# Kernel tuning notes

Hardware: AMD Instinct MI355X
Metric: run time of the kernel (lower is better)

The kernel has to match this reference:

```python
import jax, jax.numpy as jnp
import numpy as np

B_, L, D = 4, 2048, 1024          # batch, seq_len, d_model
E = 2 * D                         # d_inner (expand=2)
N = 8                             # d_state
K = 4                             # d_conv
R = D // 16                       # dt_rank = 64
EPS = 1e-5


def silu(x):
    return x * jax.nn.sigmoid(x)


def setup_inputs() -> dict:
    key = jax.random.key(0)
    ks = jax.random.split(key, 8)
    s = 0.02
    inp = jax.random.normal(ks[0], (B_, L, D), jnp.float32)
    in_proj_w = jax.random.normal(ks[1], (2 * E, D), jnp.float32) * s
    conv_w = jax.random.normal(ks[2], (E, 1, K), jnp.float32) * s  # depthwise, OIW
    conv_b = jnp.zeros((E,), jnp.float32)
    x_proj_w = jax.random.normal(ks[3], (R + 2 * N, E), jnp.float32) * s
    dt_proj_w = jax.random.normal(ks[4], (E, R), jnp.float32) * s
    # bias so softplus(dt) gives realistic small timesteps
    dt_proj_b = jax.random.uniform(ks[5], (E,), jnp.float32, minval=-4.0, maxval=-2.0)
    # S4D-real init: A = -[1..N] per channel
    A_log = jnp.log(jnp.broadcast_to(jnp.arange(1, N + 1, dtype=jnp.float32), (E, N)))
    D_param = jnp.ones((E,), jnp.float32)
    out_proj_w = jax.random.normal(ks[6], (D, E), jnp.float32) * s
    rms_w = jnp.ones((D,), jnp.float32)
    return dict(inp=inp, in_proj_w=in_proj_w, conv_w=conv_w, conv_b=conv_b,
                x_proj_w=x_proj_w, dt_proj_w=dt_proj_w, dt_proj_b=dt_proj_b,
                A_log=A_log, D_param=D_param, out_proj_w=out_proj_w, rms_w=rms_w)


def reference(inp, in_proj_w, conv_w, conv_b, x_proj_w, dt_proj_w, dt_proj_b,
              A_log, D_param, out_proj_w, rms_w):
    b, l, d = inp.shape
    # input projection -> x (ssm branch) and z (gate branch), each (b, l, E)
    xz = inp @ in_proj_w.T
    x, z = jnp.split(xz, 2, axis=-1)
    # depthwise causal conv1d along time
    xt = x.transpose(0, 2, 1)                                   # (b, E, l)
    xc = jax.lax.conv_general_dilated(xt, conv_w, (1,), [(K - 1, 0)],
                                      feature_group_count=E)
    x = silu((xc + conv_b[None, :, None]).transpose(0, 2, 1))   # (b, l, E)
    # data-dependent SSM params
    dbc = x @ x_proj_w.T                                        # (b, l, R+2N)
    dt, Bm, Cm = jnp.split(dbc, [R, R + N], axis=-1)
    delta = jax.nn.softplus(dt @ dt_proj_w.T + dt_proj_b)       # (b, l, E)
    A = -jnp.exp(A_log)                                         # (E, N)

    def step(h, t):
        d_t, B_t, C_t, u_t = t                                  # (b,E),(b,N),(b,N),(b,E)
        dA = jnp.exp(d_t[..., None] * A)                        # (b, E, N)
        h = h * dA + (d_t * u_t)[..., None] * B_t[:, None, :]
        y = jnp.einsum('ben,bn->be', h, C_t)
        return h, y

    xs = (delta.transpose(1, 0, 2), Bm.transpose(1, 0, 2),
          Cm.transpose(1, 0, 2), x.transpose(1, 0, 2))
    h0 = jnp.zeros((b, E, N), inp.dtype)
    _, ys = jax.lax.scan(step, h0, xs)                          # ys: (l, b, E)
    y = ys.transpose(1, 0, 2) + x * D_param                     # skip term u*D
    y = y * silu(z)                                             # gating
    out = y @ out_proj_w.T                                      # (b, l, D)
    # RMSNorm
    out = out * jax.lax.rsqrt(jnp.mean(out * out, axis=-1, keepdims=True) + EPS) * rms_w
    # dropout p=0 -> identity
    return out
```

## Files before the change

### kernel.cpp

```cpp
#include <hip/hip_runtime.h>

#define LL 2048
#define EE 2048
#define DD 1024
#define NC 64
#define CH 32

typedef short bf16x8 __attribute__((ext_vector_type(8)));
typedef float f32x4 __attribute__((ext_vector_type(4)));

__device__ inline float bf2f(unsigned short u) {
    union { unsigned u; float f; } v; v.u = ((unsigned)u) << 16; return v.f;
}
__device__ inline unsigned short f2bf(float f) {
    union { float f; unsigned u; } v; v.f = f;
    unsigned r = v.u + 0x7fff + ((v.u >> 16) & 1);
    return (unsigned short)(r >> 16);
}

__device__ inline void gload_lds16(const void* g, void* lds) {
    __builtin_amdgcn_global_load_lds(
        (const __attribute__((address_space(1))) unsigned int*)g,
        (__attribute__((address_space(3))) unsigned int*)lds, 16, 0, 0);
}

template<int MODE, int BN>
__global__ __launch_bounds__(512, 2)
void gemm4p(const unsigned short* __restrict__ A,
            const unsigned short* __restrict__ Bw,
            void* __restrict__ Cout,
            const float* __restrict__ bias,
            int M, int N, int K)
{
    constexpr int NREP = BN / 64;
    constexpr int RB   = BN / 128;
    constexpr int LH   = 2 + RB;
    constexpr int NSTRIP = BN / 4;

    extern __shared__ short lds[];
    short* Asm = lds;
    short* Bsm = lds + 2 * 2 * 256 * 32;

    const int tid = threadIdx.x;
    const int w = tid >> 6, lane = tid & 63;
    const int wm = w >> 2, wn = w & 3;

    const int gx = N / BN;
    const int nwg = gx * (M / 256);
    int lin = blockIdx.y * gx + blockIdx.x;
    int swz = ((nwg & 7) == 0) ? ((lin & 7) * (nwg >> 3) + (lin >> 3)) : lin;
    const long m0 = (long)(swz / gx) * 256;
    const long n0 = (long)(swz % gx) * BN;

    const int g = (tid & 3) ^ ((tid >> 3) & 3);
    const int arow = tid >> 2;
    const unsigned short* Ag = A + (m0 + arow) * (long)K + g * 8;
    const unsigned short* Bg = Bw + (n0 + arow) * (long)K + g * 8;
    const int ldsrow = w * 16;

    auto stageA = [&](int buf, int kh, int j, int kt) {
        gload_lds16(Ag + (long)j * 128 * K + kt * 64 + kh * 32,
                    Asm + ((buf * 2 + kh) * 256 + j * 128 + ldsrow) * 32);
    };
    auto stageB = [&](int buf, int kh, int j, int kt) {
        gload_lds16(Bg + (long)j * 128 * K + kt * 64 + kh * 32,
                    Bsm + ((buf * 2 + kh) * BN + j * 128 + ldsrow) * 32);
    };

    f32x4 acc[8][NREP] = {};

    stageA(0, 0, 0, 0); stageA(0, 0, 1, 0);
#pragma unroll
    for (int j = 0; j < RB; ++j) stageB(0, 0, j, 0);
    stageA(0, 1, 0, 0); stageA(0, 1, 1, 0);
#pragma unroll
    for (int j = 0; j < RB; ++j) stageB(0, 1, j, 0);
    asm volatile("s_waitcnt vmcnt(%0)" :: "i"(LH) : "memory");
    __builtin_amdgcn_s_barrier();

    const int NT = K / 64;
    const int rr = lane & 15;
    const int sl = ((lane >> 4) ^ ((rr >> 1) & 3)) * 8;

    for (int t = 0; t < NT; ++t) {
        const int cur = t & 1, nxt = cur ^ 1;
        const bool more = (t + 1 < NT);
        const short* Ac0 = Asm + (cur * 2 + 0) * 256 * 32;
        const short* Bc0 = Bsm + (cur * 2 + 0) * BN * 32;
        const short* Ac1 = Asm + (cur * 2 + 1) * 256 * 32;
        const short* Bc1 = Bsm + (cur * 2 + 1) * BN * 32;
        bf16x8 a[4], b[NREP];

#pragma unroll
        for (int n = 0; n < NREP; ++n)
            b[n] = *(const bf16x8*)&Bc0[(wn * NSTRIP + n * 16 + rr) * 32 + sl];
#pragma unroll
        for (int m = 0; m < 4; ++m)
            a[m] = *(const bf16x8*)&Ac0[(wm * 128 + m * 16 + rr) * 32 + sl];
        if (more) { stageA(nxt, 0, 0, t + 1); stageA(nxt, 0, 1, t + 1); }
        __builtin_amdgcn_s_barrier();
        asm volatile("s_waitcnt lgkmcnt(0)" ::: "memory");
        __builtin_amdgcn_sched_barrier(0);
        __builtin_amdgcn_s_setprio(1);
#pragma unroll
        for (int m = 0; m < 4; ++m)
#pragma unroll
            for (int n = 0; n < NREP; ++n)
                acc[m][n] = __builtin_amdgcn_mfma_f32_16x16x32_bf16(a[m], b[n], acc[m][n], 0, 0, 0);
        __builtin_amdgcn_s_setprio(0);
        __builtin_amdgcn_s_barrier();

#pragma unroll
        for (int m = 0; m < 4; ++m)
            a[m] = *(const bf16x8*)&Ac0[(wm * 128 + 64 + m * 16 + rr) * 32 + sl];
        if (more) {
#pragma unroll
            for (int j = 0; j < RB; ++j) stageB(nxt, 0, j, t + 1);
            asm volatile("s_waitcnt vmcnt(%0)" :: "i"(LH) : "memory");
        } else {
            asm volatile("s_waitcnt vmcnt(0)" ::: "memory");
        }
        __builtin_amdgcn_s_barrier();
        asm volatile("s_waitcnt lgkmcnt(0)" ::: "memory");
        __builtin_amdgcn_sched_barrier(0);
        __builtin_amdgcn_s_setprio(1);
#pragma unroll
        for (int m = 0; m < 4; ++m)
#pragma unroll
            for (int n = 0; n < NREP; ++n)
                acc[4 + m][n] = __builtin_amdgcn_mfma_f32_16x16x32_bf16(a[m], b[n], acc[4 + m][n], 0, 0, 0);
        __builtin_amdgcn_s_setprio(0);
        __builtin_amdgcn_s_barrier();

#pragma unroll
        for (int n = 0; n < NREP; ++n)
            b[n] = *(const bf16x8*)&Bc1[(wn * NSTRIP + n * 16 + rr) * 32 + sl];
#pragma unroll
        for (int m = 0; m < 4; ++m)
            a[m] = *(const bf16x8*)&Ac1[(wm * 128 + m * 16 + rr) * 32 + sl];
        if (more) { stageA(nxt, 1, 0, t + 1); stageA(nxt, 1, 1, t + 1); }
        __builtin_amdgcn_s_barrier();
        asm volatile("s_waitcnt lgkmcnt(0)" ::: "memory");
        __builtin_amdgcn_sched_barrier(0);
        __builtin_amdgcn_s_setprio(1);
#pragma unroll
        for (int m = 0; m < 4; ++m)
#pragma unroll
            for (int n = 0; n < NREP; ++n)
                acc[m][n] = __builtin_amdgcn_mfma_f32_16x16x32_bf16(a[m], b[n], acc[m][n], 0, 0, 0);
        __builtin_amdgcn_s_setprio(0);
        __builtin_amdgcn_s_barrier();

#pragma unroll
        for (int m = 0; m < 4; ++m)
            a[m] = *(const bf16x8*)&Ac1[(wm * 128 + 64 + m * 16 + rr) * 32 + sl];
        if (more) {
#pragma unroll
            for (int j = 0; j < RB; ++j) stageB(nxt, 1, j, t + 1);
            asm volatile("s_waitcnt vmcnt(%0)" :: "i"(LH) : "memory");
        }
        __builtin_amdgcn_s_barrier();
        asm volatile("s_waitcnt lgkmcnt(0)" ::: "memory");
        __builtin_amdgcn_sched_barrier(0);
        __builtin_amdgcn_s_setprio(1);
#pragma unroll
        for (int m = 0; m < 4; ++m)
#pragma unroll
            for (int n = 0; n < NREP; ++n)
                acc[4 + m][n] = __builtin_amdgcn_mfma_f32_16x16x32_bf16(a[m], b[n], acc[4 + m][n], 0, 0, 0);
        __builtin_amdgcn_s_setprio(0);
        __builtin_amdgcn_s_barrier();
    }

#pragma unroll
    for (int m = 0; m < 8; ++m) {
#pragma unroll
        for (int n = 0; n < NREP; ++n) {
#pragma unroll
            for (int r = 0; r < 4; ++r) {
                long row = m0 + wm * 128 + m * 16 + (lane >> 4) * 4 + r;
                long col = n0 + wn * NSTRIP + n * 16 + (lane & 15);
                float v = acc[m][n][r];
                if (MODE == 0) {
                    ((float*)Cout)[row * N + col] = v;
                } else if (MODE == 1) {
                    ((unsigned short*)Cout)[row * N + col] = f2bf(v);
                } else {
                    v += bias[col];
                    float sp = (v > 20.f) ? v : log1pf(__expf(v));
                    ((unsigned short*)Cout)[row * N + col] = f2bf(sp);
                }
            }
        }
    }
}

__global__ __launch_bounds__(256)
void gemm_xp(const unsigned short* __restrict__ A,
             const unsigned short* __restrict__ Bw,
             float* __restrict__ Cout)
{
    __shared__ short As[128 * 32];
    __shared__ short Bs[128 * 32];
    const int tid = threadIdx.x;
    const int wave = tid >> 6, lane = tid & 63;
    const int wm = wave >> 1, wn = wave & 1;
    const long m0 = (long)blockIdx.x * 128;
    const int kz = blockIdx.y;
    float* out = Cout + (long)kz * 8192 * 128;

    f32x4 acc[4][4] = {};

    const int srow = lane >> 2;
    const int g = (lane & 3) ^ ((srow >> 1) & 3);
    const int c0 = wave, c1 = wave + 4;

    for (int k0 = kz * 256; k0 < kz * 256 + 256; k0 += 32) {
        gload_lds16(A + (m0 + c0 * 16 + srow) * 2048L + k0 + g * 8, &As[c0 * 16 * 32]);
        gload_lds16(A + (m0 + c1 * 16 + srow) * 2048L + k0 + g * 8, &As[c1 * 16 * 32]);
        gload_lds16(Bw + (c0 * 16 + srow) * 2048L + k0 + g * 8, &Bs[c0 * 16 * 32]);
        gload_lds16(Bw + (c1 * 16 + srow) * 2048L + k0 + g * 8, &Bs[c1 * 16 * 32]);
        __syncthreads();

        const int rr = lane & 15;
        const int sl = ((lane >> 4) ^ ((rr >> 1) & 3)) * 8;
        bf16x8 af[4], bfr[4];
#pragma unroll
        for (int m = 0; m < 4; ++m)
            af[m] = *(const bf16x8*)&As[(wm * 64 + m * 16 + rr) * 32 + sl];
#pragma unroll
        for (int n = 0; n < 4; ++n)
            bfr[n] = *(const bf16x8*)&Bs[(wn * 64 + n * 16 + rr) * 32 + sl];
#pragma unroll
        for (int m = 0; m < 4; ++m)
#pragma unroll
            for (int n = 0; n < 4; ++n)
                acc[m][n] = __builtin_amdgcn_mfma_f32_16x16x32_bf16(af[m], bfr[n], acc[m][n], 0, 0, 0);
        __syncthreads();
    }

#pragma unroll
    for (int m = 0; m < 4; ++m)
#pragma unroll
        for (int n = 0; n < 4; ++n)
#pragma unroll
            for (int r = 0; r < 4; ++r) {
                long row = m0 + wm * 64 + m * 16 + (lane >> 4) * 4 + r;
                long col = wn * 64 + n * 16 + (lane & 15);
                out[row * 128 + col] = acc[m][n][r];
            }
}

__global__ void reduce_dbc(const float* __restrict__ part,
                           float* __restrict__ dbc,
                           unsigned short* __restrict__ dt)
{
    const long i = (long)blockIdx.x * 256 + threadIdx.x;
    float s = 0.f;
#pragma unroll
    for (int k = 0; k < 8; ++k) s += part[i + (long)k * 1048576];
    dbc[i] = s;
    const int c = (int)(i & 127);
    if (c < 64) dt[(i >> 7) * 64 + c] = f2bf(s);
}

__device__ inline void cvt4(const float* __restrict__ in, unsigned short* __restrict__ out, long i) {
    float4 v = ((const float4*)in)[i];
    unsigned lo = (unsigned)f2bf(v.x) | ((unsigned)f2bf(v.y) << 16);
    unsigned hi = (unsigned)f2bf(v.z) | ((unsigned)f2bf(v.w) << 16);
    ((uint2*)out)[i] = make_uint2(lo, hi);
}

__global__ void cvt_all(const float* __restrict__ inp, const float* __restrict__ w_in,
                        const float* __restrict__ w_xp, const float* __restrict__ w_dt,
                        const float* __restrict__ w_out,
                        unsigned short* __restrict__ o_inp, unsigned short* __restrict__ o_win,
                        unsigned short* __restrict__ o_wxp, unsigned short* __restrict__ o_wdt,
                        unsigned short* __restrict__ o_wout)
{
    const long t = (long)blockIdx.x * 256 + threadIdx.x;
    const long gs = (long)gridDim.x * 256;
    for (long i = t; i < 8388608 / 4; i += gs) cvt4(inp, o_inp, i);
    for (long i = t; i < 4194304 / 4; i += gs) cvt4(w_in, o_win, i);
    for (long i = t; i < 2097152 / 4; i += gs) cvt4(w_out, o_wout, i);
    for (long i = t; i < 131072 / 4; i += gs) cvt4(w_dt, o_wdt, i);
    for (long i = t; i < 262144 / 4; i += gs) {
        const int r = (int)(i >> 9);
        if (r < 80) cvt4(w_xp, o_wxp, i);
        else ((uint2*)o_wxp)[i] = make_uint2(0u, 0u);
    }
}

__global__ void conv_silu_k(const unsigned short* __restrict__ xz,
                            const float* __restrict__ cw,
                            const float* __restrict__ cb,
                            unsigned short* __restrict__ xc)
{
    const int ep = blockIdx.y * 256 + threadIdx.x;
    const int e0 = ep * 2, e1 = e0 + 1;
    const int b = blockIdx.z;
    const int l0 = blockIdx.x * 32;
    const float wa0 = cw[e0 * 4], wa1 = cw[e0 * 4 + 1], wa2 = cw[e0 * 4 + 2], wa3 = cw[e0 * 4 + 3];
    const float wb0 = cw[e1 * 4], wb1 = cw[e1 * 4 + 1], wb2 = cw[e1 * 4 + 2], wb3 = cw[e1 * 4 + 3];
    const float ba = cb[e0], bb = cb[e1];
    const unsigned* xrow = (const unsigned*)(xz + (long)b * LL * 4096) + ep;
    unsigned* orow = (unsigned*)(xc + (long)b * LL * 2048) + ep;

    float a3 = 0.f, a2 = 0.f, a1 = 0.f, b3 = 0.f, b2 = 0.f, b1 = 0.f;
    if (l0 >= 3) { unsigned u = xrow[(long)(l0 - 3) * 2048]; a3 = bf2f(u & 0xffff); b3 = bf2f(u >> 16); }
    if (l0 >= 2) { unsigned u = xrow[(long)(l0 - 2) * 2048]; a2 = bf2f(u & 0xffff); b2 = bf2f(u >> 16); }
    if (l0 >= 1) { unsigned u = xrow[(long)(l0 - 1) * 2048]; a1 = bf2f(u & 0xffff); b1 = bf2f(u >> 16); }
    for (int l = l0; l < l0 + 32; ++l) {
        unsigned u = xrow[(long)l * 2048];
        float xa = bf2f(u & 0xffff), xb = bf2f(u >> 16);
        float va = ba + wa0 * a3 + wa1 * a2 + wa2 * a1 + wa3 * xa;
        float vb = bb + wb0 * b3 + wb1 * b2 + wb2 * b1 + wb3 * xb;
        float sa = va / (1.f + __expf(-va));
        float sb = vb / (1.f + __expf(-vb));
        orow[(long)l * 1024] = (unsigned)f2bf(sa) | ((unsigned)f2bf(sb) << 16);
        a3 = a2; a2 = a1; a1 = xa;
        b3 = b2; b2 = b1; b1 = xb;
    }
}

__global__ __launch_bounds__(256)
void scan_local(const unsigned short* __restrict__ delta,
                const unsigned short* __restrict__ xconv,
                const float* __restrict__ dbc,
                const float* __restrict__ A_log,
                float* __restrict__ hend, float* __restrict__ Ssum)
{
    const int ep = blockIdx.x * 256 + threadIdx.x;
    const int e0 = ep * 2;
    const int c = blockIdx.y, b = blockIdx.z;
    const int l0 = c * CH;
    float An[16];
#pragma unroll
    for (int n = 0; n < 16; ++n) An[n] = -__expf(A_log[e0 * 8 + n]);
    float h[16] = {};
    float S0 = 0.f, S1 = 0.f;
    const unsigned* drow = (const unsigned*)(delta + ((long)b * LL + l0) * EE) + ep;
    const unsigned* urow = (const unsigned*)(xconv + ((long)b * LL + l0) * EE) + ep;
    const float* bc = dbc + ((long)b * LL + l0) * 128;
    for (int l = 0; l < CH; ++l) {
        unsigned dv = drow[(long)l * 1024];
        unsigned uv = urow[(long)l * 1024];
        float d0 = bf2f(dv & 0xffff), d1 = bf2f(dv >> 16);
        float u0 = bf2f(uv & 0xffff), u1 = bf2f(uv >> 16);
        float du0 = d0 * u0, du1 = d1 * u1;
        S0 += d0; S1 += d1;
#pragma unroll
        for (int n = 0; n < 8; ++n) {
            float bn = bc[l * 128 + 64 + n];
            h[n]     = h[n]     * __expf(d0 * An[n])     + du0 * bn;
            h[8 + n] = h[8 + n] * __expf(d1 * An[8 + n]) + du1 * bn;
        }
    }
    const long o = ((long)b * NC + c) * EE + e0;
#pragma unroll
    for (int n = 0; n < 8; ++n) { hend[o * 8 + n] = h[n]; hend[(o + 1) * 8 + n] = h[8 + n]; }
    Ssum[o] = S0; Ssum[o + 1] = S1;
}

__global__ __launch_bounds__(256)
void scan_combine(const float* __restrict__ hend, const float* __restrict__ Ssum,
                  const float* __restrict__ A_log, float* __restrict__ hin)
{
    const int t = blockIdx.x * 256 + threadIdx.x;
    const int b = t >> 11, e = t & 2047;
    float An[8];
#pragma unroll
    for (int n = 0; n < 8; ++n) An[n] = -__expf(A_log[e * 8 + n]);
    float h[8] = {};
    for (int c = 0; c < NC; ++c) {
        const long o = ((long)b * NC + c) * EE + e;
#pragma unroll
        for (int n = 0; n < 8; ++n) hin[o * 8 + n] = h[n];
        float S = Ssum[o];
#pragma unroll
        for (int n = 0; n < 8; ++n)
            h[n] = h[n] * __expf(An[n] * S) + hend[o * 8 + n];
    }
}

__global__ __launch_bounds__(256)
void scan_final(const unsigned short* __restrict__ delta,
                const unsigned short* __restrict__ xconv,
                const float* __restrict__ dbc,
                const unsigned short* __restrict__ xz,
                const float* __restrict__ A_log,
                const float* __restrict__ Dparam,
                const float* __restrict__ hin,
                unsigned short* __restrict__ yg)
{
    const int ep = blockIdx.x * 256 + threadIdx.x;
    const int e0 = ep * 2;
    const int c = blockIdx.y, b = blockIdx.z;
    const int l0 = c * CH;
    float An[16];
#pragma unroll
    for (int n = 0; n < 16; ++n) An[n] = -__expf(A_log[e0 * 8 + n]);
    const float Dp0 = Dparam[e0], Dp1 = Dparam[e0 + 1];
    float h[16];
    const long o = ((long)b * NC + c) * EE + e0;
#pragma unroll
    for (int n = 0; n < 8; ++n) { h[n] = hin[o * 8 + n]; h[8 + n] = hin[(o + 1) * 8 + n]; }
    const unsigned* drow = (const unsigned*)(delta + ((long)b * LL + l0) * EE) + ep;
    const unsigned* urow = (const unsigned*)(xconv + ((long)b * LL + l0) * EE) + ep;
    const unsigned* zrow = (const unsigned*)(xz + ((long)b * LL + l0) * 4096 + 2048) + ep;
    const float* bc = dbc + ((long)b * LL + l0) * 128;
    unsigned* yrow = (unsigned*)(yg + ((long)b * LL + l0) * EE) + ep;
    for (int l = 0; l < CH; ++l) {
        unsigned dv = drow[(long)l * 1024];
        unsigned uv = urow[(long)l * 1024];
        float d0 = bf2f(dv & 0xffff), d1 = bf2f(dv >> 16);
        float u0 = bf2f(uv & 0xffff), u1 = bf2f(uv >> 16);
        float du0 = d0 * u0, du1 = d1 * u1;
        float y0 = 0.f, y1 = 0.f;
#pragma unroll
        for (int n = 0; n < 8; ++n) {
            float bn = bc[l * 128 + 64 + n];
            float cn = bc[l * 128 + 72 + n];
            h[n]     = h[n]     * __expf(d0 * An[n])     + du0 * bn;
            h[8 + n] = h[8 + n] * __expf(d1 * An[8 + n]) + du1 * bn;
            y0 += h[n] * cn;
            y1 += h[8 + n] * cn;
        }
        y0 += u0 * Dp0; y1 += u1 * Dp1;
        unsigned zv = zrow[(long)l * 2048];
        float z0 = bf2f(zv & 0xffff), z1 = bf2f(zv >> 16);
        float g0 = z0 / (1.f + __expf(-z0));
        float g1 = z1 / (1.f + __expf(-z1));
        yrow[(long)l * 1024] = (unsigned)f2bf(y0 * g0) | ((unsigned)f2bf(y1 * g1) << 16);
    }
}

__global__ __launch_bounds__(256)
void rmsnorm_k(const unsigned short* __restrict__ in, const float* __restrict__ w,
               float* __restrict__ out)
{
    const int row = blockIdx.x;
    uint2 v2 = *(const uint2*)(in + (long)row * 1024 + threadIdx.x * 4);
    float x0 = bf2f(v2.x & 0xffff), x1 = bf2f(v2.x >> 16);
    float x2 = bf2f(v2.y & 0xffff), x3 = bf2f(v2.y >> 16);
    float ss = x0 * x0 + x1 * x1 + x2 * x2 + x3 * x3;
#pragma unroll
    for (int m = 32; m >= 1; m >>= 1) ss += __shfl_xor(ss, m, 64);
    __shared__ float wsum[4];
    const int wave = threadIdx.x >> 6;
    if ((threadIdx.x & 63) == 0) wsum[wave] = ss;
    __syncthreads();
    float tot = wsum[0] + wsum[1] + wsum[2] + wsum[3];
    float sc = rsqrtf(tot * (1.f / 1024.f) + 1e-5f);
    float4 wv = ((const float4*)w)[threadIdx.x];
    float4 o;
    o.x = x0 * sc * wv.x; o.y = x1 * sc * wv.y;
    o.z = x2 * sc * wv.z; o.w = x3 * sc * wv.w;
    ((float4*)(out + (long)row * 1024))[threadIdx.x] = o;
}

extern "C" void kernel_launch(void* const* d_in, const int* in_sizes, int n_in,
                              void* d_out, int out_size, void* d_ws, size_t ws_size,
                              hipStream_t stream)
{
    const float* inp   = (const float*)d_in[0];
    const float* w_in  = (const float*)d_in[1];
    const float* convw = (const float*)d_in[2];
    const float* convb = (const float*)d_in[3];
    const float* w_xp  = (const float*)d_in[4];
    const float* w_dt  = (const float*)d_in[5];
    const float* b_dt  = (const float*)d_in[6];
    const float* A_log = (const float*)d_in[7];
    const float* Dp    = (const float*)d_in[8];
    const float* w_out = (const float*)d_in[9];
    const float* rmsw  = (const float*)d_in[10];

    char* ws = (char*)d_ws;
    const size_t MB = 1024 * 1024;
    unsigned short* inp_bf   = (unsigned short*)(ws + 0);
    unsigned short* win_bf   = (unsigned short*)(ws + 16 * MB);
    unsigned short* xz_bf    = (unsigned short*)(ws + 24 * MB);
    unsigned short* xconv_bf = (unsigned short*)(ws + 88 * MB);
    unsigned short* wxp_bf   = (unsigned short*)(ws + 120 * MB);
    float*          dbc      = (float*)(ws + 121 * MB);
    unsigned short* dt_bf    = (unsigned short*)(ws + 125 * MB);
    unsigned short* wdt_bf   = (unsigned short*)(ws + 126 * MB);
    unsigned short* delta_bf = (unsigned short*)(ws + 127 * MB);
    unsigned short* yg_bf    = (unsigned short*)(ws + 191 * MB);
    unsigned short* wout_bf  = (unsigned short*)(ws + 223 * MB);
    float*          dbc_part = (float*)(ws + 159 * MB);
    float*          hend     = (float*)(ws + 159 * MB);
    float*          hin      = (float*)(ws + 175 * MB);
    float*          Ssum     = (float*)(ws + 0);
    unsigned short* out_pre  = (unsigned short*)(ws + 0);

    hipFuncSetAttribute((const void*)gemm4p<1, 256>, hipFuncAttributeMaxDynamicSharedMemorySize, 131072);
    hipFuncSetAttribute((const void*)gemm4p<2, 128>, hipFuncAttributeMaxDynamicSharedMemorySize, 98304);
    hipFuncSetAttribute((const void*)gemm4p<1, 128>, hipFuncAttributeMaxDynamicSharedMemorySize, 98304);

    cvt_all<<<2048, 256, 0, stream>>>(inp, w_in, w_xp, w_dt, w_out,
                                      inp_bf, win_bf, wxp_bf, wdt_bf, wout_bf);

    gemm4p<1, 256><<<dim3(16, 32), 512, 131072, stream>>>(inp_bf, win_bf, xz_bf, nullptr, 8192, 4096, 1024);
    conv_silu_k<<<dim3(64, 4, 4), 256, 0, stream>>>(xz_bf, convw, convb, xconv_bf);
    gemm_xp<<<dim3(64, 8), 256, 0, stream>>>(xconv_bf, wxp_bf, dbc_part);
    reduce_dbc<<<4096, 256, 0, stream>>>(dbc_part, dbc, dt_bf);
    gemm4p<2, 128><<<dim3(16, 32), 512, 98304, stream>>>(dt_bf, wdt_bf, delta_bf, b_dt, 8192, 2048, 64);
    scan_local<<<dim3(4, NC, 4), 256, 0, stream>>>(delta_bf, xconv_bf, dbc, A_log, hend, Ssum);
    scan_combine<<<32, 256, 0, stream>>>(hend, Ssum, A_log, hin);
    scan_final<<<dim3(4, NC, 4), 256, 0, stream>>>(delta_bf, xconv_bf, dbc, xz_bf, A_log, Dp, hin, yg_bf);
    gemm4p<1, 128><<<dim3(8, 32), 512, 98304, stream>>>(yg_bf, wout_bf, out_pre, nullptr, 8192, 1024, 2048);
    rmsnorm_k<<<8192, 256, 0, stream>>>(out_pre, rmsw, (float*)d_out);
}
```

Baseline: 339.0 us.

## Restructure GEMM barrier schedule, add small dt GEMM, parallelize scan combine

The main GEMM loop is reorganized to use one vmcnt wait and barrier per half-K step instead of several barriers per quarter-step. Prefetch issue is interleaved with MFMA blocks, and the explicit lgkmcnt waits and sched barriers are dropped. The K=64 delta projection moves to a dedicated 128x128 tile kernel with a fused softplus epilogue. gemm_xp uses fewer split-K partitions with a matching reduce, and scan_combine maps one thread per state element, giving 8x more threads. Fewer barriers risk LDS races or worse compiler scheduling, since the compiler now places the LDS waits itself.

```diff
diff --git a/kernel.cpp b/kernel.cpp
--- a/kernel.cpp
+++ b/kernel.cpp
@@ -26,10 +26,9 @@
 
 template<int MODE, int BN>
 __global__ __launch_bounds__(512, 2)
-void gemm4p(const unsigned short* __restrict__ A,
+void gemm8p(const unsigned short* __restrict__ A,
             const unsigned short* __restrict__ Bw,
             void* __restrict__ Cout,
-            const float* __restrict__ bias,
             int M, int N, int K)
 {
     constexpr int NREP = BN / 64;
@@ -75,8 +74,6 @@
     stageA(0, 1, 0, 0); stageA(0, 1, 1, 0);
 #pragma unroll
     for (int j = 0; j < RB; ++j) stageB(0, 1, j, 0);
-    asm volatile("s_waitcnt vmcnt(%0)" :: "i"(LH) : "memory");
-    __builtin_amdgcn_s_barrier();
 
     const int NT = K / 64;
     const int rr = lane & 15;
@@ -85,22 +82,20 @@
     for (int t = 0; t < NT; ++t) {
         const int cur = t & 1, nxt = cur ^ 1;
         const bool more = (t + 1 < NT);
+
+        asm volatile("s_waitcnt vmcnt(%0)" :: "i"(LH) : "memory");
+        __builtin_amdgcn_s_barrier();
+
         const short* Ac0 = Asm + (cur * 2 + 0) * 256 * 32;
         const short* Bc0 = Bsm + (cur * 2 + 0) * BN * 32;
-        const short* Ac1 = Asm + (cur * 2 + 1) * 256 * 32;
-        const short* Bc1 = Bsm + (cur * 2 + 1) * BN * 32;
+        if (more) { stageA(nxt, 0, 0, t + 1); stageA(nxt, 0, 1, t + 1); }
         bf16x8 a[4], b[NREP];
-
+#pragma unroll
+        for (int m = 0; m < 4; ++m)
+            a[m] = *(const bf16x8*)&Ac0[(wm * 128 + m * 16 + rr) * 32 + sl];
 #pragma unroll
         for (int n = 0; n < NREP; ++n)
             b[n] = *(const bf16x8*)&Bc0[(wn * NSTRIP + n * 16 + rr) * 32 + sl];
-#pragma unroll
-        for (int m = 0; m < 4; ++m)
-            a[m] = *(const bf16x8*)&Ac0[(wm * 128 + m * 16 + rr) * 32 + sl];
-        if (more) { stageA(nxt, 0, 0, t + 1); stageA(nxt, 0, 1, t + 1); }
-        __builtin_amdgcn_s_barrier();
-        asm volatile("s_waitcnt lgkmcnt(0)" ::: "memory");
-        __builtin_amdgcn_sched_barrier(0);
         __builtin_amdgcn_s_setprio(1);
 #pragma unroll
         for (int m = 0; m < 4; ++m)
@@ -108,21 +103,13 @@
             for (int n = 0; n < NREP; ++n)
                 acc[m][n] = __builtin_amdgcn_mfma_f32_16x16x32_bf16(a[m], b[n], acc[m][n], 0, 0, 0);
         __builtin_amdgcn_s_setprio(0);
-        __builtin_amdgcn_s_barrier();
-
+        if (more) {
+#pragma unroll
+            for (int j = 0; j < RB; ++j) stageB(nxt, 0, j, t + 1);
+        }
 #pragma unroll
         for (int m = 0; m < 4; ++m)
             a[m] = *(const bf16x8*)&Ac0[(wm * 128 + 64 + m * 16 + rr) * 32 + sl];
-        if (more) {
-#pragma unroll
-            for (int j = 0; j < RB; ++j) stageB(nxt, 0, j, t + 1);
-            asm volatile("s_waitcnt vmcnt(%0)" :: "i"(LH) : "memory");
-        } else {
-            asm volatile("s_waitcnt vmcnt(0)" ::: "memory");
-        }
-        __builtin_amdgcn_s_barrier();
-        asm volatile("s_waitcnt lgkmcnt(0)" ::: "memory");
-        __builtin_amdgcn_sched_barrier(0);
         __builtin_amdgcn_s_setprio(1);
 #pragma unroll
         for (int m = 0; m < 4; ++m)
@@ -130,18 +117,20 @@
             for (int n = 0; n < NREP; ++n)
                 acc[4 + m][n] = __builtin_amdgcn_mfma_f32_16x16x32_bf16(a[m], b[n], acc[4 + m][n], 0, 0, 0);
         __builtin_amdgcn_s_setprio(0);
+
+        if (more) { asm volatile("s_waitcnt vmcnt(%0)" :: "i"(LH) : "memory"); }
+        else      { asm volatile("s_waitcnt vmcnt(0)" ::: "memory"); }
         __builtin_amdgcn_s_barrier();
 
+        const short* Ac1 = Asm + (cur * 2 + 1) * 256 * 32;
+        const short* Bc1 = Bsm + (cur * 2 + 1) * BN * 32;
+        if (more) { stageA(nxt, 1, 0, t + 1); stageA(nxt, 1, 1, t + 1); }
+#pragma unroll
+        for (int m = 0; m < 4; ++m)
+            a[m] = *(const bf16x8*)&Ac1[(wm * 128 + m * 16 + rr) * 32 + sl];
 #pragma unroll
         for (int n = 0; n < NREP; ++n)
             b[n] = *(const bf16x8*)&Bc1[(wn * NSTRIP + n * 16 + rr) * 32 + sl];
-#pragma unroll
-        for (int m = 0; m < 4; ++m)
-            a[m] = *(const bf16x8*)&Ac1[(wm * 128 + m * 16 + rr) * 32 + sl];
-        if (more) { stageA(nxt, 1, 0, t + 1); stageA(nxt, 1, 1, t + 1); }
-        __builtin_amdgcn_s_barrier();
-        asm volatile("s_waitcnt lgkmcnt(0)" ::: "memory");
-        __builtin_amdgcn_sched_barrier(0);
         __builtin_amdgcn_s_setprio(1);
 #pragma unroll
         for (int m = 0; m < 4; ++m)
@@ -149,19 +138,13 @@
             for (int n = 0; n < NREP; ++n)
                 acc[m][n] = __builtin_amdgcn_mfma_f32_16x16x32_bf16(a[m], b[n], acc[m][n], 0, 0, 0);
         __builtin_amdgcn_s_setprio(0);
-        __builtin_amdgcn_s_barrier();
-
+        if (more) {
+#pragma unroll
+            for (int j = 0; j < RB; ++j) stageB(nxt, 1, j, t + 1);
+        }
 #pragma unroll
         for (int m = 0; m < 4; ++m)
             a[m] = *(const bf16x8*)&Ac1[(wm * 128 + 64 + m * 16 + rr) * 32 + sl];
-        if (more) {
-#pragma unroll
-            for (int j = 0; j < RB; ++j) stageB(nxt, 1, j, t + 1);
-            asm volatile("s_waitcnt vmcnt(%0)" :: "i"(LH) : "memory");
-        }
-        __builtin_amdgcn_s_barrier();
-        asm volatile("s_waitcnt lgkmcnt(0)" ::: "memory");
-        __builtin_amdgcn_sched_barrier(0);
         __builtin_amdgcn_s_setprio(1);
 #pragma unroll
         for (int m = 0; m < 4; ++m)
@@ -169,7 +152,6 @@
             for (int n = 0; n < NREP; ++n)
                 acc[4 + m][n] = __builtin_amdgcn_mfma_f32_16x16x32_bf16(a[m], b[n], acc[4 + m][n], 0, 0, 0);
         __builtin_amdgcn_s_setprio(0);
-        __builtin_amdgcn_s_barrier();
     }
 
 #pragma unroll
@@ -181,15 +163,8 @@
                 long row = m0 + wm * 128 + m * 16 + (lane >> 4) * 4 + r;
                 long col = n0 + wn * NSTRIP + n * 16 + (lane & 15);
                 float v = acc[m][n][r];
-                if (MODE == 0) {
-                    ((float*)Cout)[row * N + col] = v;
-                } else if (MODE == 1) {
-                    ((unsigned short*)Cout)[row * N + col] = f2bf(v);
-                } else {
-                    v += bias[col];
-                    float sp = (v > 20.f) ? v : log1pf(__expf(v));
-                    ((unsigned short*)Cout)[row * N + col] = f2bf(sp);
-                }
+                if (MODE == 0) ((float*)Cout)[row * N + col] = v;
+                else           ((unsigned short*)Cout)[row * N + col] = f2bf(v);
             }
         }
     }
@@ -215,7 +190,7 @@
     const int g = (lane & 3) ^ ((srow >> 1) & 3);
     const int c0 = wave, c1 = wave + 4;
 
-    for (int k0 = kz * 256; k0 < kz * 256 + 256; k0 += 32) {
+    for (int k0 = kz * 512; k0 < kz * 512 + 512; k0 += 32) {
         gload_lds16(A + (m0 + c0 * 16 + srow) * 2048L + k0 + g * 8, &As[c0 * 16 * 32]);
         gload_lds16(A + (m0 + c1 * 16 + srow) * 2048L + k0 + g * 8, &As[c1 * 16 * 32]);
         gload_lds16(Bw + (c0 * 16 + srow) * 2048L + k0 + g * 8, &Bs[c0 * 16 * 32]);
@@ -256,12 +231,68 @@
                            unsigned short* __restrict__ dt)
 {
     const long i = (long)blockIdx.x * 256 + threadIdx.x;
-    float s = 0.f;
-#pragma unroll
-    for (int k = 0; k < 8; ++k) s += part[i + (long)k * 1048576];
+    float s = part[i] + part[i + 1048576] + part[i + 2 * 1048576] + part[i + 3 * 1048576];
     dbc[i] = s;
     const int c = (int)(i & 127);
     if (c < 64) dt[(i >> 7) * 64 + c] = f2bf(s);
+}
+
+__global__ __launch_bounds__(256)
+void gemm_dt(const unsigned short* __restrict__ A,
+             const unsigned short* __restrict__ Bw,
+             const float* __restrict__ bias,
+             unsigned short* __restrict__ Cout)
+{
+    __shared__ short As[128 * 32];
+    __shared__ short Bs[128 * 32];
+    const int tid = threadIdx.x;
+    const int wave = tid >> 6, lane = tid & 63;
+    const int wm = wave >> 1, wn = wave & 1;
+    const long m0 = (long)blockIdx.y * 128;
+    const long n0 = (long)blockIdx.x * 128;
+
+    f32x4 acc[4][4] = {};
+
+    const int srow = lane >> 2;
+    const int g = (lane & 3) ^ ((srow >> 1) & 3);
+    const int c0 = wave, c1 = wave + 4;
+
+    for (int k0 = 0; k0 < 64; k0 += 32) {
+        gload_lds16(A + (m0 + c0 * 16 + srow) * 64L + k0 + g * 8, &As[c0 * 16 * 32]);
+        gload_lds16(A + (m0 + c1 * 16 + srow) * 64L + k0 + g * 8, &As[c1 * 16 * 32]);
+        gload_lds16(Bw + (n0 + c0 * 16 + srow) * 64L + k0 + g * 8, &Bs[c0 * 16 * 32]);
+        gload_lds16(Bw + (n0 + c1 * 16 + srow) * 64L + k0 + g * 8, &Bs[c1 * 16 * 32]);
+        __syncthreads();
+
+        const int rr = lane & 15;
+        const int sl = ((lane >> 4) ^ ((rr >> 1) & 3)) * 8;
+        bf16x8 af[4], bfr[4];
+#pragma unroll
+        for (int m = 0; m < 4; ++m)
+            af[m] = *(const bf16x8*)&As[(wm * 64 + m * 16 + rr) * 32 + sl];
+#pragma unroll
+        for (int n = 0; n < 4; ++n)
+            bfr[n] = *(const bf16x8*)&Bs[(wn * 64 + n * 16 + rr) * 32 + sl];
+#pragma unroll
+        for (int m = 0; m < 4; ++m)
+#pragma unroll
+            for (int n = 0; n < 4; ++n)
+                acc[m][n] = __builtin_amdgcn_mfma_f32_16x16x32_bf16(af[m], bfr[n], acc[m][n], 0, 0, 0);
+        __syncthreads();
+    }
+
+#pragma unroll
+    for (int m = 0; m < 4; ++m)
+#pragma unroll
+        for (int n = 0; n < 4; ++n)
+#pragma unroll
+            for (int r = 0; r < 4; ++r) {
+                long row = m0 + wm * 64 + m * 16 + (lane >> 4) * 4 + r;
+                long col = n0 + wn * 64 + n * 16 + (lane & 15);
+                float v = acc[m][n][r] + bias[col];
+                float sp = (v > 20.f) ? v : log1pf(__expf(v));
+                Cout[row * 2048 + col] = f2bf(sp);
+            }
 }
 
 __device__ inline void cvt4(const float* __restrict__ in, unsigned short* __restrict__ out, long i) {
@@ -367,19 +398,15 @@
                   const float* __restrict__ A_log, float* __restrict__ hin)
 {
     const int t = blockIdx.x * 256 + threadIdx.x;
-    const int b = t >> 11, e = t & 2047;
-    float An[8];
-#pragma unroll
-    for (int n = 0; n < 8; ++n) An[n] = -__expf(A_log[e * 8 + n]);
-    float h[8] = {};
+    const int n = t & 7;
+    const int be = t >> 3;
+    const int b = be >> 11, e = be & 2047;
+    const float An = -__expf(A_log[e * 8 + n]);
+    float h = 0.f;
     for (int c = 0; c < NC; ++c) {
         const long o = ((long)b * NC + c) * EE + e;
-#pragma unroll
-        for (int n = 0; n < 8; ++n) hin[o * 8 + n] = h[n];
-        float S = Ssum[o];
-#pragma unroll
-        for (int n = 0; n < 8; ++n)
-            h[n] = h[n] * __expf(An[n] * S) + hend[o * 8 + n];
+        hin[o * 8 + n] = h;
+        h = h * __expf(An * Ssum[o]) + hend[o * 8 + n];
     }
 }
 
@@ -494,21 +521,20 @@
     float*          Ssum     = (float*)(ws + 0);
     unsigned short* out_pre  = (unsigned short*)(ws + 0);
 
-    hipFuncSetAttribute((const void*)gemm4p<1, 256>, hipFuncAttributeMaxDynamicSharedMemorySize, 131072);
-    hipFuncSetAttribute((const void*)gemm4p<2, 128>, hipFuncAttributeMaxDynamicSharedMemorySize, 98304);
-    hipFuncSetAttribute((const void*)gemm4p<1, 128>, hipFuncAttributeMaxDynamicSharedMemorySize, 98304);
+    hipFuncSetAttribute((const void*)gemm8p<1, 256>, hipFuncAttributeMaxDynamicSharedMemorySize, 131072);
+    hipFuncSetAttribute((const void*)gemm8p<1, 128>, hipFuncAttributeMaxDynamicSharedMemorySize, 98304);
 
     cvt_all<<<2048, 256, 0, stream>>>(inp, w_in, w_xp, w_dt, w_out,
                                       inp_bf, win_bf, wxp_bf, wdt_bf, wout_bf);
 
-    gemm4p<1, 256><<<dim3(16, 32), 512, 131072, stream>>>(inp_bf, win_bf, xz_bf, nullptr, 8192, 4096, 1024);
+    gemm8p<1, 256><<<dim3(16, 32), 512, 131072, stream>>>(inp_bf, win_bf, xz_bf, 8192, 4096, 1024);
     conv_silu_k<<<dim3(64, 4, 4), 256, 0, stream>>>(xz_bf, convw, convb, xconv_bf);
-    gemm_xp<<<dim3(64, 8), 256, 0, stream>>>(xconv_bf, wxp_bf, dbc_part);
+    gemm_xp<<<dim3(64, 4), 256, 0, stream>>>(xconv_bf, wxp_bf, dbc_part);
     reduce_dbc<<<4096, 256, 0, stream>>>(dbc_part, dbc, dt_bf);
-    gemm4p<2, 128><<<dim3(16, 32), 512, 98304, stream>>>(dt_bf, wdt_bf, delta_bf, b_dt, 8192, 2048, 64);
+    gemm_dt<<<dim3(16, 64), 256, 0, stream>>>(dt_bf, wdt_bf, b_dt, delta_bf);
     scan_local<<<dim3(4, NC, 4), 256, 0, stream>>>(delta_bf, xconv_bf, dbc, A_log, hend, Ssum);
-    scan_combine<<<32, 256, 0, stream>>>(hend, Ssum, A_log, hin);
+    scan_combine<<<256, 256, 0, stream>>>(hend, Ssum, A_log, hin);
     scan_final<<<dim3(4, NC, 4), 256, 0, stream>>>(delta_bf, xconv_bf, dbc, xz_bf, A_log, Dp, hin, yg_bf);
-    gemm4p<1, 128><<<dim3(8, 32), 512, 98304, stream>>>(yg_bf, wout_bf, out_pre, nullptr, 8192, 1024, 2048);
+    gemm8p<1, 128><<<dim3(8, 32), 512, 98304, stream>>>(yg_bf, wout_bf, out_pre, 8192, 1024, 2048);
     rmsnorm_k<<<8192, 256, 0, stream>>>(out_pre, rmsw, (float*)d_out);
 }
```

New measurement: 323.4 us. -4.6%, faster.
